# Optimization experiments

Measured on AMD Instinct MI355X. Metric: run time of the kernel, lower is better.

Reference implementation:

```python
import jax, jax.numpy as jnp
import numpy as np

T, H, L, OUT = 100, 100, 5, 10  # seq_len, hidden/input dim, n_lstm_layers, output dim


def _lstm_layer(x, Wih, Whh, bih, bhh):
    """Single-layer LSTM, PyTorch gate order (i, f, g, o).
    x: [T, B, H] -> outputs [T, B, H]. Zero initial state."""
    B = x.shape[1]
    b = bih + bhh  # [4H]
    # precompute input contributions for all timesteps: [T, B, 4H]
    xg = jnp.einsum('tbi,gi->tbg', x, Wih) + b

    def step(carry, xg_t):
        h, c = carry
        gates = xg_t + h @ Whh.T  # [B, 4H]
        i, f, g, o = jnp.split(gates, 4, axis=-1)
        i = jax.nn.sigmoid(i)
        f = jax.nn.sigmoid(f)
        g = jnp.tanh(g)
        o = jax.nn.sigmoid(o)
        c = f * c + i * g
        h = o * jnp.tanh(c)
        return (h, c), h

    h0 = jnp.zeros((B, H), dtype=x.dtype)
    c0 = jnp.zeros((B, H), dtype=x.dtype)
    _, ys = jax.lax.scan(step, (h0, c0), xg)
    return ys  # [T, B, H]


def setup_inputs() -> dict:
    key = jax.random.key(0)
    ks = jax.random.split(key, 7)
    s = 0.1
    return {
        'input': jax.random.normal(ks[0], (1, T, H), dtype=jnp.float32),
        'Wih': jax.random.normal(ks[1], (L, 4 * H, H), dtype=jnp.float32) * s,
        'Whh': jax.random.normal(ks[2], (L, 4 * H, H), dtype=jnp.float32) * s,
        'bih': jax.random.normal(ks[3], (L, 4 * H), dtype=jnp.float32) * s,
        'bhh': jax.random.normal(ks[4], (L, 4 * H), dtype=jnp.float32) * s,
        'W_out': jax.random.normal(ks[5], (OUT, H), dtype=jnp.float32) * s,
        'b_out': jax.random.normal(ks[6], (OUT,), dtype=jnp.float32) * s,
    }


def reference(input, Wih, Whh, bih, bhh, W_out, b_out):
    # batch_first [B, T, H] -> time-major [T, B, H] for scan
    x = jnp.transpose(input.reshape(-1, T, H), (1, 0, 2))
    for l in range(L):
        x = _lstm_layer(x, Wih[l], Whh[l], bih[l], bhh[l])
        if l < L - 1:
            x = jax.nn.relu(x)  # inter-layer ReLU (not after last LSTM)
    out = jax.nn.sigmoid(x @ W_out.T + b_out)  # [T, B, OUT]
    return jnp.transpose(out, (1, 0, 2)).reshape(T, OUT)
```

## Files before the change

kernel.cpp:

```cpp
#include <hip/hip_runtime.h>

#define TT 100
#define HH 100
#define NL 5
#define NOUT 10
#define NG 400
#define CC 10
#define NC (TT / CC)

__device__ __forceinline__ float fast_sigmoid(float x) {
  return 1.f / (1.f + __expf(-x));
}
__device__ __forceinline__ float fast_tanh(float x) {
  float xc = fminf(fmaxf(x, -9.f), 9.f);
  float e2 = __expf(2.f * xc);
  return (e2 - 1.f) / (e2 + 1.f);
}

__launch_bounds__(512, 2)
__global__ void lstm_pipe_kernel(
    const float* __restrict__ input,
    const float* __restrict__ Wih,
    const float* __restrict__ Whh,
    const float* __restrict__ bih,
    const float* __restrict__ bhh,
    const float* __restrict__ Wout,
    const float* __restrict__ bout,
    float* __restrict__ out,
    int* __restrict__ flags,
    float* __restrict__ xstage)
{
  const int l = blockIdx.x;
  const int tid = threadIdx.x;

  __shared__ __align__(16) float xch[CC * HH];
  __shared__ __align__(16) float och[CC * HH];
  __shared__ __align__(16) float hbuf[HH];
  __shared__ __align__(16) float gact[NG];
  __shared__ __align__(16) float pacc[256];

  float4 wv[25];
  float4 uv[25];
  float bias = 0.0f;

  if (tid < NG) {
    const float4* wr = (const float4*)(Wih + (size_t)l * NG * HH + (size_t)tid * HH);
    const float4* ur = (const float4*)(Whh + (size_t)l * NG * HH + (size_t)tid * HH);
#pragma unroll 25
    for (int k = 0; k < 25; ++k) wv[k] = wr[k];
#pragma unroll 25
    for (int k = 0; k < 25; ++k) uv[k] = ur[k];
    bias = bih[l * NG + tid] + bhh[l * NG + tid];
  }

  float4 wo = make_float4(0.f, 0.f, 0.f, 0.f);
  float bo = 0.f;
  if (l == NL - 1) {
    if (tid < 250) {
      int row = tid / 25, kq = tid % 25;
      wo = ((const float4*)(Wout + row * HH))[kq];
    }
    if (tid < NOUT) bo = bout[tid];
  }

  float c = 0.f;
  if (tid < HH) hbuf[tid] = 0.f;
  __syncthreads();

  for (int ch = 0; ch < NC; ++ch) {
    if (l == 0) {
      if (tid < CC * HH / 4)
        ((float4*)xch)[tid] = ((const float4*)(input + ch * CC * HH))[tid];
    } else {
      const int* fl = flags + (l - 1) * NC + ch;
      while (__hip_atomic_load(fl, __ATOMIC_ACQUIRE, __HIP_MEMORY_SCOPE_AGENT) == 0) {
      }
      const float4* src =
          (const float4*)(xstage + ((size_t)(l - 1) * TT + (size_t)ch * CC) * HH);
      if (tid < CC * HH / 4) ((float4*)xch)[tid] = src[tid];
    }
    __syncthreads();

    for (int s = 0; s < CC; ++s) {
      if (tid < NG) {
        float acc = bias;
        const float4* x4 = (const float4*)(xch + s * HH);
        const float4* h4 = (const float4*)hbuf;
#pragma unroll 25
        for (int k = 0; k < 25; ++k) {
          float4 xv = x4[k];
          acc = fmaf(wv[k].x, xv.x, acc);
          acc = fmaf(wv[k].y, xv.y, acc);
          acc = fmaf(wv[k].z, xv.z, acc);
          acc = fmaf(wv[k].w, xv.w, acc);
        }
#pragma unroll 25
        for (int k = 0; k < 25; ++k) {
          float4 hv = h4[k];
          acc = fmaf(uv[k].x, hv.x, acc);
          acc = fmaf(uv[k].y, hv.y, acc);
          acc = fmaf(uv[k].z, hv.z, acc);
          acc = fmaf(uv[k].w, hv.w, acc);
        }
        gact[tid] = (tid < 2 * HH || tid >= 3 * HH) ? fast_sigmoid(acc)
                                                    : fast_tanh(acc);
      }
      __syncthreads();

      if (tid < HH) {
        float ig = gact[tid];
        float fg = gact[HH + tid];
        float gg = gact[2 * HH + tid];
        float og = gact[3 * HH + tid];
        c = fg * c + ig * gg;
        float h = og * fast_tanh(c);
        hbuf[tid] = h;
        if (l < NL - 1) och[s * HH + tid] = fmaxf(h, 0.f);
      }
      __syncthreads();

      if (l == NL - 1) {
        if (tid < 250) {
          int kq = tid % 25;
          const float4* h4 = (const float4*)hbuf;
          float4 hv = h4[kq];
          pacc[tid] = wo.x * hv.x + wo.y * hv.y + wo.z * hv.z + wo.w * hv.w;
        }
        __syncthreads();
        if (tid < NOUT) {
          float ssum = bo;
#pragma unroll 25
          for (int p = 0; p < 25; ++p) ssum += pacc[tid * 25 + p];
          out[(ch * CC + s) * NOUT + tid] = fast_sigmoid(ssum);
        }
      }
    }

    if (l < NL - 1) {
      float4* dst = (float4*)(xstage + ((size_t)l * TT + (size_t)ch * CC) * HH);
      if (tid < CC * HH / 4) dst[tid] = ((const float4*)och)[tid];
      __syncthreads();
      if (tid == 0) {
        __threadfence();
        __hip_atomic_store(flags + l * NC + ch, 1, __ATOMIC_RELEASE,
                           __HIP_MEMORY_SCOPE_AGENT);
      }
    }
  }
}

extern "C" void kernel_launch(void* const* d_in, const int* in_sizes, int n_in,
                              void* d_out, int out_size, void* d_ws, size_t ws_size,
                              hipStream_t stream) {
  const float* input = (const float*)d_in[0];
  const float* Wih   = (const float*)d_in[1];
  const float* Whh   = (const float*)d_in[2];
  const float* bih   = (const float*)d_in[3];
  const float* bhh   = (const float*)d_in[4];
  const float* Wout  = (const float*)d_in[5];
  const float* bout  = (const float*)d_in[6];
  float* out = (float*)d_out;

  int* flags = (int*)d_ws;
  float* xstage = (float*)((char*)d_ws + 2048);

  hipMemsetAsync(d_ws, 0, 2048, stream);

  lstm_pipe_kernel<<<dim3(NL), dim3(512), 0, stream>>>(
      input, Wih, Whh, bih, bhh, Wout, bout, out, flags, xstage);
}
```

Measured before the change: 225.5 us.

## Precompute chunk input projections, interleave gates per lane with shuffles, batch output projection

Reorders the gate rows so the four gates of each hidden unit sit in adjacent lanes, which lets the cell update use cross-lane shuffles instead of a shared gate buffer and an extra barrier. The input projection for a whole chunk of timesteps is computed up front from the Wih rows streamed out of global memory, so the recurrent step only runs the Whh dot product, with packed v2f FMAs over split accumulators. The h buffer is double-buffered so each step needs one barrier, and the output projection is done once per chunk instead of once per step. Other changes: tanh is written through sigmoid, the spin-wait sleeps, and launch bounds drop to one block per CU. The risks are more register pressure from the per-chunk accumulators and reloading Wih from global memory for every chunk.

Measured after the change: 259.9 us. 15.3% more time.

```diff
diff --git a/kernel.cpp b/kernel.cpp
--- a/kernel.cpp
+++ b/kernel.cpp
@@ -8,16 +8,11 @@
 #define CC 10
 #define NC (TT / CC)
 
-__device__ __forceinline__ float fast_sigmoid(float x) {
-  return 1.f / (1.f + __expf(-x));
-}
-__device__ __forceinline__ float fast_tanh(float x) {
-  float xc = fminf(fmaxf(x, -9.f), 9.f);
-  float e2 = __expf(2.f * xc);
-  return (e2 - 1.f) / (e2 + 1.f);
-}
+typedef float v2f __attribute__((ext_vector_type(2)));
 
-__launch_bounds__(512, 2)
+__device__ __forceinline__ float sigm(float x) { return 1.f / (1.f + __expf(-x)); }
+
+__launch_bounds__(512, 1)
 __global__ void lstm_pipe_kernel(
     const float* __restrict__ input,
     const float* __restrict__ Wih,
@@ -32,40 +27,26 @@
 {
   const int l = blockIdx.x;
   const int tid = threadIdx.x;
+  const int j = tid >> 2;
+  const int g = tid & 3;
+  const int row = g * HH + j;
 
   __shared__ __align__(16) float xch[CC * HH];
   __shared__ __align__(16) float och[CC * HH];
-  __shared__ __align__(16) float hbuf[HH];
-  __shared__ __align__(16) float gact[NG];
-  __shared__ __align__(16) float pacc[256];
+  __shared__ __align__(16) float hbuf[2][HH];
 
-  float4 wv[25];
-  float4 uv[25];
-  float bias = 0.0f;
-
+  v2f uv[50];
+  float bias = 0.f;
   if (tid < NG) {
-    const float4* wr = (const float4*)(Wih + (size_t)l * NG * HH + (size_t)tid * HH);
-    const float4* ur = (const float4*)(Whh + (size_t)l * NG * HH + (size_t)tid * HH);
-#pragma unroll 25
-    for (int k = 0; k < 25; ++k) wv[k] = wr[k];
-#pragma unroll 25
-    for (int k = 0; k < 25; ++k) uv[k] = ur[k];
-    bias = bih[l * NG + tid] + bhh[l * NG + tid];
+    const v2f* ur = (const v2f*)(Whh + (size_t)l * NG * HH + (size_t)row * HH);
+#pragma unroll
+    for (int k = 0; k < 50; ++k) uv[k] = ur[k];
+    bias = bih[l * NG + row] + bhh[l * NG + row];
   }
-
-  float4 wo = make_float4(0.f, 0.f, 0.f, 0.f);
-  float bo = 0.f;
-  if (l == NL - 1) {
-    if (tid < 250) {
-      int row = tid / 25, kq = tid % 25;
-      wo = ((const float4*)(Wout + row * HH))[kq];
-    }
-    if (tid < NOUT) bo = bout[tid];
-  }
+  const float4* wr = (const float4*)(Wih + (size_t)l * NG * HH + (size_t)row * HH);
 
   float c = 0.f;
-  if (tid < HH) hbuf[tid] = 0.f;
-  __syncthreads();
+  if (tid < HH) hbuf[0][tid] = 0.f;
 
   for (int ch = 0; ch < NC; ++ch) {
     if (l == 0) {
@@ -73,68 +54,77 @@
         ((float4*)xch)[tid] = ((const float4*)(input + ch * CC * HH))[tid];
     } else {
       const int* fl = flags + (l - 1) * NC + ch;
-      while (__hip_atomic_load(fl, __ATOMIC_ACQUIRE, __HIP_MEMORY_SCOPE_AGENT) == 0) {
-      }
+      while (__hip_atomic_load(fl, __ATOMIC_ACQUIRE, __HIP_MEMORY_SCOPE_AGENT) == 0)
+        __builtin_amdgcn_s_sleep(1);
       const float4* src =
           (const float4*)(xstage + ((size_t)(l - 1) * TT + (size_t)ch * CC) * HH);
       if (tid < CC * HH / 4) ((float4*)xch)[tid] = src[tid];
     }
     __syncthreads();
 
+    float xgr[CC];
+    if (tid < NG) {
+      v2f acc[2 * CC];
+#pragma unroll
+      for (int s = 0; s < 2 * CC; ++s) acc[s] = (v2f){0.f, 0.f};
+#pragma unroll 5
+      for (int k = 0; k < 25; ++k) {
+        float4 w4 = wr[k];
+        v2f wA = {w4.x, w4.y}, wB = {w4.z, w4.w};
+#pragma unroll
+        for (int s = 0; s < CC; ++s) {
+          float4 xv = ((const float4*)xch)[s * 25 + k];
+          v2f xA = {xv.x, xv.y}, xB = {xv.z, xv.w};
+          acc[2 * s] = wA * xA + acc[2 * s];
+          acc[2 * s + 1] = wB * xB + acc[2 * s + 1];
+        }
+      }
+#pragma unroll
+      for (int s = 0; s < CC; ++s) {
+        v2f t = acc[2 * s] + acc[2 * s + 1];
+        xgr[s] = bias + t.x + t.y;
+      }
+    }
+
+#pragma unroll
     for (int s = 0; s < CC; ++s) {
+      __syncthreads();
       if (tid < NG) {
-        float acc = bias;
-        const float4* x4 = (const float4*)(xch + s * HH);
-        const float4* h4 = (const float4*)hbuf;
-#pragma unroll 25
-        for (int k = 0; k < 25; ++k) {
-          float4 xv = x4[k];
-          acc = fmaf(wv[k].x, xv.x, acc);
-          acc = fmaf(wv[k].y, xv.y, acc);
-          acc = fmaf(wv[k].z, xv.z, acc);
-          acc = fmaf(wv[k].w, xv.w, acc);
-        }
-#pragma unroll 25
+        const float4* h4 = (const float4*)hbuf[s & 1];
+        v2f a0 = {xgr[s], 0.f}, a1 = {0.f, 0.f}, a2 = {0.f, 0.f}, a3 = {0.f, 0.f};
+#pragma unroll
         for (int k = 0; k < 25; ++k) {
           float4 hv = h4[k];
-          acc = fmaf(uv[k].x, hv.x, acc);
-          acc = fmaf(uv[k].y, hv.y, acc);
-          acc = fmaf(uv[k].z, hv.z, acc);
-          acc = fmaf(uv[k].w, hv.w, acc);
+          v2f hA = {hv.x, hv.y}, hB = {hv.z, hv.w};
+          if (k & 1) {
+            a2 = uv[2 * k] * hA + a2;
+            a3 = uv[2 * k + 1] * hB + a3;
+          } else {
+            a0 = uv[2 * k] * hA + a0;
+            a1 = uv[2 * k + 1] * hB + a1;
+          }
         }
-        gact[tid] = (tid < 2 * HH || tid >= 3 * HH) ? fast_sigmoid(acc)
-                                                    : fast_tanh(acc);
-      }
-      __syncthreads();
+        v2f t = (a0 + a2) + (a1 + a3);
+        float a = t.x + t.y;
 
-      if (tid < HH) {
-        float ig = gact[tid];
-        float fg = gact[HH + tid];
-        float gg = gact[2 * HH + tid];
-        float og = gact[3 * HH + tid];
-        c = fg * c + ig * gg;
-        float h = og * fast_tanh(c);
-        hbuf[tid] = h;
-        if (l < NL - 1) och[s * HH + tid] = fmaxf(h, 0.f);
-      }
-      __syncthreads();
+        bool isg = (g == 2);
+        float m = isg ? 2.f : 1.f;
+        float sg = 1.f / (1.f + __expf(-m * a));
+        float v = isg ? 2.f * sg - 1.f : sg;
 
-      if (l == NL - 1) {
-        if (tid < 250) {
-          int kq = tid % 25;
-          const float4* h4 = (const float4*)hbuf;
-          float4 hv = h4[kq];
-          pacc[tid] = wo.x * hv.x + wo.y * hv.y + wo.z * hv.z + wo.w * hv.w;
-        }
-        __syncthreads();
-        if (tid < NOUT) {
-          float ssum = bo;
-#pragma unroll 25
-          for (int p = 0; p < 25; ++p) ssum += pacc[tid * 25 + p];
-          out[(ch * CC + s) * NOUT + tid] = fast_sigmoid(ssum);
+        float v1 = __shfl_xor(v, 1);
+        float v2v = __shfl_xor(v, 2);
+        float v3 = __shfl_xor(v1, 2);
+        if (g == 0) {
+          c = v1 * c + v * v2v;
+          float tc = 2.f / (1.f + __expf(-2.f * c)) - 1.f;
+          float h = v3 * tc;
+          hbuf[(s + 1) & 1][j] = h;
+          och[s * HH + j] = (l < NL - 1) ? fmaxf(h, 0.f) : h;
         }
       }
     }
+    __syncthreads();
 
     if (l < NL - 1) {
       float4* dst = (float4*)(xstage + ((size_t)l * TT + (size_t)ch * CC) * HH);
@@ -145,6 +135,20 @@
         __hip_atomic_store(flags + l * NC + ch, 1, __ATOMIC_RELEASE,
                            __HIP_MEMORY_SCOPE_AGENT);
       }
+    } else {
+      if (tid < NG) {
+        int p = tid >> 2, q = tid & 3;
+        int s2 = p / 10, r = p % 10;
+        const float* wrow = Wout + r * HH + q * 25;
+        const float* hrow = och + s2 * HH + q * 25;
+        float acc = 0.f;
+#pragma unroll
+        for (int m2 = 0; m2 < 25; ++m2) acc = fmaf(wrow[m2], hrow[m2], acc);
+        acc += __shfl_xor(acc, 1);
+        acc += __shfl_xor(acc, 2);
+        if (q == 0) out[(ch * CC + s2) * NOUT + r] = sigm(acc + bout[r]);
+      }
+      __syncthreads();
     }
   }
 }
```
